# Performance work log

Hardware: AMD Instinct MI355X
Metric: run time of the kernel (lower is better)

The kernel has to match this reference:

```python
import jax, jax.numpy as jnp
import numpy as np
from jax import lax

HEADS, DIM_HEAD, LANDMARKS, PINV_ITERS = 8, 64, 256, 6
D = 512


def layernorm(x, w, b, eps=1e-5):
    mu = x.mean(-1, keepdims=True)
    var = ((x - mu) ** 2).mean(-1, keepdims=True)
    return (x - mu) * lax.rsqrt(var + eps) * w + b


def pinv_iter(x, iters=PINV_ITERS):
    # Moore-Penrose pseudo-inverse via Newton-Schulz (lucidrains nystrom-attention)
    abs_x = jnp.abs(x)
    z = jnp.swapaxes(x, -1, -2) / (jnp.max(abs_x.sum(-1)) * jnp.max(abs_x.sum(-2)))
    I = jnp.eye(x.shape[-1], dtype=x.dtype)
    for _ in range(iters):
        xz = x @ z
        z = 0.25 * z @ (13 * I - xz @ (15 * I - xz @ (7 * I - xz)))
    return z


def nystrom_attention(x, qkv_w, out_w, out_b, res_w):
    b, n, _ = x.shape
    m = LANDMARKS
    pad = (m - n % m) % m
    xp = jnp.pad(x, ((0, 0), (pad, 0), (0, 0)))  # left-pad seq to multiple of m
    n_p = n + pad
    q, k, v = jnp.split(xp @ qkv_w, 3, axis=-1)
    split = lambda t: t.reshape(b, n_p, HEADS, DIM_HEAD).transpose(0, 2, 1, 3)
    q, k, v = split(q), split(k), split(v)  # (b, h, n_p, d)
    q = q * DIM_HEAD ** -0.5
    l = n_p // m  # tokens per landmark
    q_l = q.reshape(b, HEADS, m, l, DIM_HEAD).mean(3)  # (b, h, m, d)
    k_l = k.reshape(b, HEADS, m, l, DIM_HEAD).mean(3)
    a1 = jax.nn.softmax(jnp.einsum('bhnd,bhmd->bhnm', q, k_l), -1)  # (b,h,n_p,m)
    a2 = jax.nn.softmax(jnp.einsum('bhmd,bhld->bhml', q_l, k_l), -1)  # (b,h,m,m)
    a3 = jax.nn.softmax(jnp.einsum('bhmd,bhnd->bhmn', q_l, k), -1)  # (b,h,m,n_p)
    out = (a1 @ pinv_iter(a2)) @ (a3 @ v)  # (b,h,n_p,d)
    # depthwise residual conv over the seq dim, kernel (33,1), one per head
    res = lax.conv_general_dilated(v, res_w, (1, 1), [(16, 16), (0, 0)],
                                   dimension_numbers=('NCHW', 'OIHW', 'NCHW'),
                                   feature_group_count=HEADS)
    out = out + res
    out = out.transpose(0, 2, 1, 3).reshape(b, n_p, HEADS * DIM_HEAD)
    return (out @ out_w + out_b)[:, -n:]


def ppeg(x, Hh, Ww, w7, b7, w5, b5, w3, b3):
    B, _, C = x.shape
    cls_tok, feat = x[:, :1], x[:, 1:]
    f = feat.transpose(0, 2, 1).reshape(B, C, Hh, Ww)
    def dwconv(w, bb, p):
        return lax.conv_general_dilated(f, w, (1, 1), [(p, p), (p, p)],
                                        dimension_numbers=('NCHW', 'OIHW', 'NCHW'),
                                        feature_group_count=C) + bb[None, :, None, None]
    y = f + dwconv(w7, b7, 3) + dwconv(w5, b5, 2) + dwconv(w3, b3, 1)
    y = y.reshape(B, C, Hh * Ww).transpose(0, 2, 1)
    return jnp.concatenate([cls_tok, y], axis=1)


def setup_inputs() -> dict:
    key = jax.random.key(0)
    ks = jax.random.split(key, 16)
    E, NC, H = 1024, 4, HEADS
    f32 = jnp.float32
    rn = lambda k, shp, s=0.02: (jax.random.normal(k, shp, f32) * s)
    return {
        'x': jax.random.normal(ks[0], (1, 40960, E), f32),
        'fc1_w': rn(ks[1], (E, D)), 'fc1_b': jnp.zeros((D,), f32),
        'cls_token': jax.random.normal(ks[2], (1, 1, D), f32),
        'l1_norm_w': jnp.ones((D,), f32), 'l1_norm_b': jnp.zeros((D,), f32),
        'l1_qkv_w': rn(ks[3], (D, 3 * D)),
        'l1_out_w': rn(ks[4], (D, D)), 'l1_out_b': jnp.zeros((D,), f32),
        'l1_res_w': rn(ks[5], (H, 1, 33, 1), 0.1),
        'ppeg_w7': rn(ks[6], (D, 1, 7, 7), 0.1), 'ppeg_b7': jnp.zeros((D,), f32),
        'ppeg_w5': rn(ks[7], (D, 1, 5, 5), 0.1), 'ppeg_b5': jnp.zeros((D,), f32),
        'ppeg_w3': rn(ks[8], (D, 1, 3, 3), 0.1), 'ppeg_b3': jnp.zeros((D,), f32),
        'l2_norm_w': jnp.ones((D,), f32), 'l2_norm_b': jnp.zeros((D,), f32),
        'l2_qkv_w': rn(ks[9], (D, 3 * D)),
        'l2_out_w': rn(ks[10], (D, D)), 'l2_out_b': jnp.zeros((D,), f32),
        'l2_res_w': rn(ks[11], (H, 1, 33, 1), 0.1),
        'norm_w': jnp.ones((D,), f32), 'norm_b': jnp.zeros((D,), f32),
        'fc3_w': rn(ks[12], (D, NC)), 'fc3_b': jnp.zeros((NC,), f32),
    }


def reference(x, fc1_w, fc1_b, cls_token, l1_norm_w, l1_norm_b, l1_qkv_w, l1_out_w, l1_out_b, l1_res_w, ppeg_w7, ppeg_b7, ppeg_w5, ppeg_b5, ppeg_w3, ppeg_b3, l2_norm_w, l2_norm_b, l2_qkv_w, l2_out_w, l2_out_b, l2_res_w, norm_w, norm_b, fc3_w, fc3_b):
    B, N, E = x.shape  # (1, 40960, 1024)
    POOL_OUT = 20480
    # AdaptiveMaxPool2d((20480, E)) on a (1, N, E) tensor: max-pool seq dim N -> 20480
    ft = x.reshape(B, POOL_OUT, N // POOL_OUT, E).max(axis=2)
    ft = jax.nn.relu(ft @ fc1_w + fc1_b)  # (1, 20480, 512)
    Hn = ft.shape[1]
    _H = int(np.ceil(np.sqrt(Hn)))  # 144
    add = _H * _H - Hn  # 256
    ft = jnp.concatenate([ft, ft[:, :add]], axis=1)  # (1, 20736, 512)
    h = jnp.concatenate([jnp.broadcast_to(cls_token, (B, 1, D)), ft], axis=1)  # 20737 tokens
    h = h + nystrom_attention(layernorm(h, l1_norm_w, l1_norm_b), l1_qkv_w, l1_out_w, l1_out_b, l1_res_w)
    h = ppeg(h, _H, _H, ppeg_w7, ppeg_b7, ppeg_w5, ppeg_b5, ppeg_w3, ppeg_b3)
    h = h + nystrom_attention(layernorm(h, l2_norm_w, l2_norm_b), l2_qkv_w, l2_out_w, l2_out_b, l2_res_w)
    h = layernorm(h, norm_w, norm_b)[:, 0]
    logits = h @ fc3_w + fc3_b
    return logits, jax.nn.softmax(logits, -1), jnp.argmax(logits, -1)
```

## Files before the change

kernel.cpp:

```cpp
#include <hip/hip_runtime.h>


constexpr int D_    = 512;
constexpr int E_    = 1024;
constexpr int NTOK  = 20737;
constexpr int NP_   = 20992;
constexpr int NH_   = 8;
constexpr int HD_   = 64;
constexpr int MLM   = 256;
constexpr int LCH   = 82;
constexpr int HHW   = 144;
constexpr int NFEAT = 20736;
constexpr int PADR  = 255;
constexpr int NCH   = 41;
constexpr int CHTOK = 512;

typedef __attribute__((ext_vector_type(8))) short bf16x8;
typedef __attribute__((ext_vector_type(4))) float f32x4;

__device__ __forceinline__ unsigned short f2bf(float f){
  unsigned int u = __float_as_uint(f);
  unsigned int r = u + 0x7fffu + ((u >> 16) & 1u);
  return (unsigned short)(r >> 16);
}
__device__ __forceinline__ float bfu(unsigned short u){
  return __uint_as_float((unsigned int)u << 16);
}

__device__ __forceinline__ float waveMaxF(float v){
#pragma unroll
  for (int o = 32; o > 0; o >>= 1) v = fmaxf(v, __shfl_xor(v, o));
  return v;
}
__device__ __forceinline__ float waveSumF(float v){
#pragma unroll
  for (int o = 32; o > 0; o >>= 1) v += __shfl_xor(v, o);
  return v;
}
__device__ __forceinline__ float blockMax256(float v, float* sbuf){
  v = waveMaxF(v);
  if ((threadIdx.x & 63) == 0) sbuf[threadIdx.x >> 6] = v;
  __syncthreads();
  float r = fmaxf(fmaxf(sbuf[0], sbuf[1]), fmaxf(sbuf[2], sbuf[3]));
  __syncthreads();
  return r;
}
__device__ __forceinline__ float blockSum256(float v, float* sbuf){
  v = waveSumF(v);
  if ((threadIdx.x & 63) == 0) sbuf[threadIdx.x >> 6] = v;
  __syncthreads();
  float r = sbuf[0] + sbuf[1] + sbuf[2] + sbuf[3];
  __syncthreads();
  return r;
}

__global__ __launch_bounds__(256) void wtrans_kernel(
    const float* __restrict__ W, unsigned short* __restrict__ Wt, int K, int N){
  __shared__ float tile[32][33];
  const int kb = blockIdx.x * 32, nb = blockIdx.y * 32;
  const int tx = threadIdx.x, ty = threadIdx.y;
  for (int i = ty; i < 32; i += 8) tile[i][tx] = W[(size_t)(kb + i) * N + nb + tx];
  __syncthreads();
  for (int i = ty; i < 32; i += 8)
    Wt[(size_t)(nb + i) * K + kb + tx] = f2bf(tile[tx][i]);
}

__global__ __launch_bounds__(256) void pool_bf16_kernel(
    const float* __restrict__ x, unsigned short* __restrict__ Ah){
  size_t idx4 = ((size_t)blockIdx.x * 256 + threadIdx.x) * 4;
  size_t m = idx4 >> 10, e = idx4 & 1023;
  float4 a = *(const float4*)(x + (m * 2) * E_ + e);
  float4 b = *(const float4*)(x + (m * 2 + 1) * E_ + e);
  unsigned long long pk =
      (unsigned long long)f2bf(fmaxf(a.x, b.x))
    | ((unsigned long long)f2bf(fmaxf(a.y, b.y)) << 16)
    | ((unsigned long long)f2bf(fmaxf(a.z, b.z)) << 32)
    | ((unsigned long long)f2bf(fmaxf(a.w, b.w)) << 48);
  *(unsigned long long*)(Ah + idx4) = pk;
}

__device__ __forceinline__ void mfma_tile128(
    const unsigned short* __restrict__ A, int arows, int bm,
    const unsigned short* __restrict__ Bt, int bn, int K,
    f32x4 acc[4][4], unsigned short* As, unsigned short* Bs){
  const int t = threadIdx.x;
  const int lane = t & 63, wave = t >> 6;
  const int wr = wave >> 1, wc = wave & 1;
  const int m16 = lane & 15, quad = lane >> 4;
  for (int kc = 0; kc < K; kc += 64){
    for (int idx = t; idx < 1024; idx += 256){
      int row = idx >> 3, off = (idx & 7) * 8;
      int ga = bm + row;
      ulonglong2 av = {0ull, 0ull};
      if (ga < arows) av = *(const ulonglong2*)(A + (size_t)ga * K + kc + off);
      *(ulonglong2*)(As + row * 72 + off) = av;
      ulonglong2 bv = *(const ulonglong2*)(Bt + (size_t)(bn + row) * K + kc + off);
      *(ulonglong2*)(Bs + row * 72 + off) = bv;
    }
    __syncthreads();
#pragma unroll
    for (int k2 = 0; k2 < 64; k2 += 32){
      bf16x8 af[4], bf[4];
#pragma unroll
      for (int mi = 0; mi < 4; mi++)
        af[mi] = *(const bf16x8*)(As + (wr * 64 + mi * 16 + m16) * 72 + k2 + quad * 8);
#pragma unroll
      for (int ni = 0; ni < 4; ni++)
        bf[ni] = *(const bf16x8*)(Bs + (wc * 64 + ni * 16 + m16) * 72 + k2 + quad * 8);
#pragma unroll
      for (int mi = 0; mi < 4; mi++)
#pragma unroll
        for (int ni = 0; ni < 4; ni++)
          acc[mi][ni] = __builtin_amdgcn_mfma_f32_16x16x32_bf16(af[mi], bf[ni], acc[mi][ni], 0, 0, 0);
    }
    __syncthreads();
  }
}

__global__ __launch_bounds__(256) void fc1_mfma_kernel(
    const unsigned short* __restrict__ Ah, const unsigned short* __restrict__ Bt,
    const float* __restrict__ bias, float* __restrict__ h){
  __shared__ unsigned short As[128 * 72], Bs[128 * 72];
  f32x4 z4 = {0.f, 0.f, 0.f, 0.f};
  f32x4 acc[4][4];
#pragma unroll
  for (int i = 0; i < 4; i++)
#pragma unroll
    for (int j = 0; j < 4; j++) acc[i][j] = z4;
  const int bm = blockIdx.x * 128, bn = blockIdx.y * 128;
  mfma_tile128(Ah, 20480, bm, Bt, bn, E_, acc, As, Bs);
  const int lane = threadIdx.x & 63, wave = threadIdx.x >> 6;
  const int wr = wave >> 1, wc = wave & 1;
  const int m16 = lane & 15, quad = lane >> 4;
#pragma unroll
  for (int mi = 0; mi < 4; mi++)
#pragma unroll
    for (int ni = 0; ni < 4; ni++){
      int col = bn + wc * 64 + ni * 16 + m16;
      float bv = bias[col];
#pragma unroll
      for (int r = 0; r < 4; r++){
        int row = bm + wr * 64 + mi * 16 + quad * 4 + r;
        float vv = fmaxf(acc[mi][ni][r] + bv, 0.f);
        h[(size_t)(1 + row) * D_ + col] = vv;
        if (row < 256) h[(size_t)(20481 + row) * D_ + col] = vv;
      }
    }
}

__global__ void cls_kernel(const float* __restrict__ cls, float* __restrict__ h){
  int c = blockIdx.x * 256 + threadIdx.x;
  if (c < D_) h[c] = cls[c];
}

__global__ void row0_copy_kernel(const float* __restrict__ src, float* __restrict__ dst){
  int c = blockIdx.x * 256 + threadIdx.x;
  if (c < D_) dst[c] = src[c];
}

__global__ __launch_bounds__(256) void ln_pad_kernel(
    const float* __restrict__ h, const float* __restrict__ w,
    const float* __restrict__ b, unsigned short* __restrict__ xph){
  const int r = blockIdx.x;
  const int t = threadIdx.x;
  if (r < PADR){
    xph[(size_t)r * D_ + t] = 0;
    xph[(size_t)r * D_ + 256 + t] = 0;
    return;
  }
  __shared__ float s4[4];
  const float* x = h + (size_t)(r - PADR) * D_;
  float a0 = x[t], a1 = x[t + 256];
  float mu = blockSum256(a0 + a1, s4) * (1.f / 512.f);
  float d0 = a0 - mu, d1 = a1 - mu;
  float var = blockSum256(d0 * d0 + d1 * d1, s4) * (1.f / 512.f);
  float rs = rsqrtf(var + 1e-5f);
  xph[(size_t)r * D_ + t]       = f2bf(d0 * rs * w[t] + b[t]);
  xph[(size_t)r * D_ + 256 + t] = f2bf(d1 * rs * w[t + 256] + b[t + 256]);
}

__global__ __launch_bounds__(256) void qkv_mfma_kernel(
    const unsigned short* __restrict__ A, const unsigned short* __restrict__ Bt,
    unsigned short* __restrict__ q16, unsigned short* __restrict__ k16,
    unsigned short* __restrict__ v16){
  __shared__ unsigned short As[128 * 72], Bs[128 * 72];
  f32x4 z4 = {0.f, 0.f, 0.f, 0.f};
  f32x4 acc[4][4];
#pragma unroll
  for (int i = 0; i < 4; i++)
#pragma unroll
    for (int j = 0; j < 4; j++) acc[i][j] = z4;
  const int bm = blockIdx.x * 128, bn = blockIdx.y * 128;
  mfma_tile128(A, NP_, bm, Bt, bn, D_, acc, As, Bs);
  const int lane = threadIdx.x & 63, wave = threadIdx.x >> 6;
  const int wr = wave >> 1, wc = wave & 1;
  const int m16 = lane & 15, quad = lane >> 4;
#pragma unroll
  for (int mi = 0; mi < 4; mi++)
#pragma unroll
    for (int ni = 0; ni < 4; ni++){
      int col = bn + wc * 64 + ni * 16 + m16;
      int which = col >> 9, hh = (col >> 6) & 7, d = col & 63;
      size_t cbase = (size_t)hh * NP_ * HD_ + d;
      unsigned short* dst;
      float sc = 1.f;
      if (which == 0){ dst = q16; sc = 0.125f; }
      else if (which == 1) dst = k16;
      else dst = v16;
#pragma unroll
      for (int r = 0; r < 4; r++){
        int row = bm + wr * 64 + mi * 16 + quad * 4 + r;
        dst[cbase + (size_t)row * HD_] = f2bf(acc[mi][ni][r] * sc);
      }
    }
}

__global__ __launch_bounds__(64) void landmark_kernel(
    const unsigned short* __restrict__ q16, const unsigned short* __restrict__ k16,
    float* __restrict__ ql, float* __restrict__ kl,
    unsigned short* __restrict__ qlh, unsigned short* __restrict__ klh){
  const int im = blockIdx.x, h = blockIdx.y, d = threadIdx.x;
  size_t base = ((size_t)h * NP_ + (size_t)im * LCH) * HD_ + d;
  float sq = 0.f, sk = 0.f;
  for (int r = 0; r < LCH; r++){
    sq += bfu(q16[base + (size_t)r * HD_]);
    sk += bfu(k16[base + (size_t)r * HD_]);
  }
  float qm = sq * (1.f / 82.f), km = sk * (1.f / 82.f);
  size_t oidx = ((size_t)h * MLM + im) * HD_ + d;
  ql[oidx] = qm;  qlh[oidx] = f2bf(qm);
  kl[oidx] = km;  klh[oidx] = f2bf(km);
}

__global__ __launch_bounds__(256) void a2_kernel(
    const float* __restrict__ ql, const float* __restrict__ kl,
    float* __restrict__ a2){
  const int im = blockIdx.x, h = blockIdx.y, t = threadIdx.x;
  __shared__ __align__(16) float qs[64];
  __shared__ float s4[4];
  if (t < 64) qs[t] = ql[((size_t)h * MLM + im) * HD_ + t];
  __syncthreads();
  const float4* kr4 = (const float4*)(kl + ((size_t)h * MLM + t) * HD_);
  const float4* qs4 = (const float4*)qs;
  float s = 0.f;
#pragma unroll
  for (int d4 = 0; d4 < 16; d4++){
    float4 kv = kr4[d4], qv = qs4[d4];
    s += qv.x*kv.x + qv.y*kv.y + qv.z*kv.z + qv.w*kv.w;
  }
  float mx = blockMax256(s, s4);
  float e = __expf(s - mx);
  float S = blockSum256(e, s4);
  a2[((size_t)h * MLM + im) * MLM + t] = e / S;
}

__global__ __launch_bounds__(256) void pinv_scale_kernel(
    const float* __restrict__ a2, float* __restrict__ scal){
  const int h = blockIdx.x, j = threadIdx.x;
  const float* A = a2 + (size_t)h * MLM * MLM;
  float rs = 0.f, cs = 0.f;
  for (int t = 0; t < MLM; t++){
    rs += fabsf(A[(size_t)j * MLM + t]);
    cs += fabsf(A[(size_t)t * MLM + j]);
  }
  __shared__ float s4[4];
  float rmax = blockMax256(rs, s4);
  float cmax = blockMax256(cs, s4);
  if (j == 0){ scal[h * 2] = rmax; scal[h * 2 + 1] = cmax; }
}

__global__ __launch_bounds__(256) void pinv_init_kernel(
    const float* __restrict__ a2, const float* __restrict__ scal,
    float* __restrict__ z){
  const int i = blockIdx.x, h = blockIdx.y, j = threadIdx.x;
  float rmax = scal[0], cmax = scal[1];
#pragma unroll
  for (int hh = 1; hh < 8; hh++){
    rmax = fmaxf(rmax, scal[hh * 2]);
    cmax = fmaxf(cmax, scal[hh * 2 + 1]);
  }
  float inv = 1.f / (rmax * cmax);
  z[((size_t)h * MLM + i) * MLM + j] = a2[((size_t)h * MLM + j) * MLM + i] * inv;
}

__global__ __launch_bounds__(256) void bmm256_mfma_kernel(
    const float* __restrict__ Ab, const float* __restrict__ Bb,
    float* __restrict__ Cb, float c0, float sgn, float c1){
  __shared__ unsigned short Ash[64 * 40], Asl[64 * 40];
  __shared__ unsigned short Bsh[64 * 40], Bsl[64 * 40];
  const int h = blockIdx.z;
  const float* A = Ab + (size_t)h * 65536;
  const float* B = Bb + (size_t)h * 65536;
  float* C = Cb + (size_t)h * 65536;
  const int bm = blockIdx.x * 64, bn = blockIdx.y * 64;
  const int t = threadIdx.x, lane = t & 63, w = t >> 6;
  const int wr = w >> 1, wc = w & 1, m16 = lane & 15, quad = lane >> 4;
  f32x4 z4 = {0.f, 0.f, 0.f, 0.f};
  f32x4 acc[2][2] = {{z4, z4}, {z4, z4}};
  for (int kc = 0; kc < 256; kc += 32){
    {
      int row = t >> 2, c8 = (t & 3) * 8;
      const float* src = A + (size_t)(bm + row) * 256 + kc + c8;
      float xs[8];
      *(float4*)(xs)     = *(const float4*)src;
      *(float4*)(xs + 4) = *(const float4*)(src + 4);
#pragma unroll
      for (int j = 0; j < 8; j++){
        unsigned short hi = f2bf(xs[j]);
        Ash[row * 40 + c8 + j] = hi;
        Asl[row * 40 + c8 + j] = f2bf(xs[j] - bfu(hi));
      }
      int k = t >> 3, n8 = (t & 7) * 8;
      const float* bsrc = B + (size_t)(kc + k) * 256 + bn + n8;
      float ys[8];
      *(float4*)(ys)     = *(const float4*)bsrc;
      *(float4*)(ys + 4) = *(const float4*)(bsrc + 4);
#pragma unroll
      for (int j = 0; j < 8; j++){
        float xv = sgn * ys[j];
        if (kc + k == bn + n8 + j) xv += c0;
        unsigned short hi = f2bf(xv);
        Bsh[(n8 + j) * 40 + k] = hi;
        Bsl[(n8 + j) * 40 + k] = f2bf(xv - bfu(hi));
      }
    }
    __syncthreads();
    bf16x8 ah[2], al[2], bh[2], bl[2];
#pragma unroll
    for (int mi = 0; mi < 2; mi++){
      ah[mi] = *(const bf16x8*)(Ash + (wr * 32 + mi * 16 + m16) * 40 + quad * 8);
      al[mi] = *(const bf16x8*)(Asl + (wr * 32 + mi * 16 + m16) * 40 + quad * 8);
      bh[mi] = *(const bf16x8*)(Bsh + (wc * 32 + mi * 16 + m16) * 40 + quad * 8);
      bl[mi] = *(const bf16x8*)(Bsl + (wc * 32 + mi * 16 + m16) * 40 + quad * 8);
    }
#pragma unroll
    for (int mi = 0; mi < 2; mi++)
#pragma unroll
      for (int ni = 0; ni < 2; ni++){
        acc[mi][ni] = __builtin_amdgcn_mfma_f32_16x16x32_bf16(ah[mi], bh[ni], acc[mi][ni], 0, 0, 0);
        acc[mi][ni] = __builtin_amdgcn_mfma_f32_16x16x32_bf16(ah[mi], bl[ni], acc[mi][ni], 0, 0, 0);
        acc[mi][ni] = __builtin_amdgcn_mfma_f32_16x16x32_bf16(al[mi], bh[ni], acc[mi][ni], 0, 0, 0);
      }
    __syncthreads();
  }
#pragma unroll
  for (int mi = 0; mi < 2; mi++)
#pragma unroll
    for (int ni = 0; ni < 2; ni++)
#pragma unroll
      for (int r = 0; r < 4; r++){
        int row = bm + wr * 32 + mi * 16 + quad * 4 + r;
        int col = bn + wc * 32 + ni * 16 + m16;
        C[(size_t)row * 256 + col] = c1 * acc[mi][ni][r];
      }
}

__global__ __launch_bounds__(256) void a3v_part_kernel(
    const unsigned short* __restrict__ qlh, const unsigned short* __restrict__ k16,
    const unsigned short* __restrict__ v16, float* __restrict__ pacc,
    float* __restrict__ pml){
  __shared__ __align__(16) unsigned short qs16[64 * 72];
  __shared__ __align__(16) unsigned short kb16[64 * 72];
  __shared__ __align__(16) unsigned short vt16[64 * 72];
  const int lt = blockIdx.x, h = blockIdx.y, ch = blockIdx.z;
  const int t = threadIdx.x;
  const int lane = t & 63, w = t >> 6;
  const int m16 = lane & 15, quad = lane >> 4;

  const unsigned short* qg = qlh + ((size_t)h * MLM + lt * 64) * HD_;
  for (int idx = t; idx < 512; idx += 256){
    int row = idx >> 3, off = (idx & 7) * 8;
    *(uint4*)(qs16 + row * 72 + off) = *(const uint4*)(qg + (size_t)row * HD_ + off);
  }
  f32x4 z4 = {0.f, 0.f, 0.f, 0.f};
  f32x4 acc_o[4] = {z4, z4, z4, z4};
  float mreg[4], lreg[4];
#pragma unroll
  for (int r = 0; r < 4; r++){ mreg[r] = -3.0e38f; lreg[r] = 0.f; }
  const unsigned short* kg = k16 + ((size_t)h * NP_ + ch * CHTOK) * HD_;
  const unsigned short* vg = v16 + ((size_t)h * NP_ + ch * CHTOK) * HD_;

  for (int sc = 0; sc < 8; sc++){
    __syncthreads();
    for (int idx = t; idx < 512; idx += 256){
      int row = idx >> 3, off = (idx & 7) * 8;
      *(uint4*)(kb16 + row * 72 + off) =
          *(const uint4*)(kg + (size_t)(sc * 64 + row) * HD_ + off);
      uint4 pv = *(const uint4*)(vg + (size_t)(sc * 64 + row) * HD_ + off);
      unsigned int uu[4] = {pv.x, pv.y, pv.z, pv.w};
#pragma unroll
      for (int j = 0; j < 4; j++){
        vt16[(off + 2 * j)     * 72 + row] = (unsigned short)(uu[j] & 0xffffu);
        vt16[(off + 2 * j + 1) * 72 + row] = (unsigned short)(uu[j] >> 16);
      }
    }
    __syncthreads();
    f32x4 acc_s[4] = {z4, z4, z4, z4};
#pragma unroll
    for (int kc = 0; kc < 64; kc += 32){
      bf16x8 a = *(const bf16x8*)(qs16 + (w * 16 + m16) * 72 + kc + quad * 8);
#pragma unroll
      for (int ni = 0; ni < 4; ni++){
        bf16x8 b = *(const bf16x8*)(kb16 + (ni * 16 + m16) * 72 + kc + quad * 8);
        acc_s[ni] = __builtin_amdgcn_mfma_f32_16x16x32_bf16(a, b, acc_s[ni], 0, 0, 0);
      }
    }
    __syncthreads();
#pragma unroll
    for (int r = 0; r < 4; r++){
      float cm = fmaxf(fmaxf(acc_s[0][r], acc_s[1][r]), fmaxf(acc_s[2][r], acc_s[3][r]));
#pragma unroll
      for (int o = 1; o < 16; o <<= 1) cm = fmaxf(cm, __shfl_xor(cm, o));
      float mn = fmaxf(mreg[r], cm);
      float scl = __expf(mreg[r] - mn);
      float p0 = __expf(acc_s[0][r] - mn), p1 = __expf(acc_s[1][r] - mn);
      float p2 = __expf(acc_s[2][r] - mn), p3 = __expf(acc_s[3][r] - mn);
      float ls = (p0 + p1) + (p2 + p3);
#pragma unroll
      for (int o = 1; o < 16; o <<= 1) ls += __shfl_xor(ls, o);
      lreg[r] = lreg[r] * scl + ls;
      mreg[r] = mn;
      acc_o[0][r] *= scl; acc_o[1][r] *= scl;
      acc_o[2][r] *= scl; acc_o[3][r] *= scl;
      int prow = (w * 16 + quad * 4 + r) * 72 + m16;
      kb16[prow + 0]  = f2bf(p0);
      kb16[prow + 16] = f2bf(p1);
      kb16[prow + 32] = f2bf(p2);
      kb16[prow + 48] = f2bf(p3);
    }
    __syncthreads();
#pragma unroll
    for (int kc = 0; kc < 64; kc += 32){
      bf16x8 a = *(const bf16x8*)(kb16 + (w * 16 + m16) * 72 + kc + quad * 8);
#pragma unroll
      for (int ni = 0; ni < 4; ni++){
        bf16x8 b = *(const bf16x8*)(vt16 + (ni * 16 + m16) * 72 + kc + quad * 8);
        acc_o[ni] = __builtin_amdgcn_mfma_f32_16x16x32_bf16(a, b, acc_o[ni], 0, 0, 0);
      }
    }
  }
#pragma unroll
  for (int r = 0; r < 4; r++){
    int im = lt * 64 + w * 16 + quad * 4 + r;
    size_t base = ((size_t)h * NCH + ch) * MLM + im;
#pragma unroll
    for (int ni = 0; ni < 4; ni++)
      pacc[base * HD_ + ni * 16 + m16] = acc_o[ni][r];
    if (m16 == 0){
      pml[base * 2]     = mreg[r];
      pml[base * 2 + 1] = lreg[r];
    }
  }
}

__global__ __launch_bounds__(64) void a3v_combine_kernel(
    const float* __restrict__ pacc, const float* __restrict__ pml,
    float* __restrict__ t1){
  const int im = blockIdx.x, h = blockIdx.y, lane = threadIdx.x;
  float M = -3.0e38f;
  for (int c = 0; c < NCH; c++)
    M = fmaxf(M, pml[(((size_t)h * NCH + c) * MLM + im) * 2]);
  float accv = 0.f, L = 0.f;
  for (int c = 0; c < NCH; c++){
    size_t base = ((size_t)h * NCH + c) * MLM + im;
    float mc = pml[base * 2], lc = pml[base * 2 + 1];
    float w = __expf(mc - M);
    accv += w * pacc[base * HD_ + lane];
    L += w * lc;
  }
  t1[((size_t)h * MLM + im) * HD_ + lane] = accv / L;
}

__global__ __launch_bounds__(256) void zt1_kernel(
    const float* __restrict__ z, const float* __restrict__ t1,
    unsigned short* __restrict__ t2t){
  const int h = blockIdx.y;
  const int t = threadIdx.x;
  const int d = t & 63, ri = t >> 6;
  const int im = blockIdx.x * 4 + ri;
  const float* zr = z + ((size_t)h * MLM + im) * MLM;
  const float* t1h = t1 + (size_t)h * MLM * HD_;
  float acc = 0.f;
#pragma unroll 8
  for (int kk = 0; kk < MLM; kk++) acc += zr[kk] * t1h[(size_t)kk * HD_ + d];
  t2t[((size_t)h * HD_ + d) * MLM + im] = f2bf(acc);
}

__global__ __launch_bounds__(256) void out_tile_kernel(
    const unsigned short* __restrict__ q16, const unsigned short* __restrict__ klh,
    const unsigned short* __restrict__ t2t, const unsigned short* __restrict__ v16,
    const float* __restrict__ resw, unsigned short* __restrict__ outh){
  __shared__ __align__(16) unsigned short smem[64 * 72 * 2 + 64 * 264];
  unsigned short* qs16 = smem;
  unsigned short* kb16 = smem + 64 * 72;
  unsigned short* Ps   = smem + 64 * 72 * 2;
  const int tile = blockIdx.x, h = blockIdx.y;
  const int n0 = PADR + tile * 64;
  const int t = threadIdx.x;
  const int lane = t & 63, w = t >> 6;
  const int m16 = lane & 15, quad = lane >> 4;

  {
    const unsigned short* qh = q16 + (size_t)h * NP_ * HD_;
    for (int idx = t; idx < 512; idx += 256){
      int row = idx >> 3, off = (idx & 7) * 8;
      int n = n0 + row;
      uint4 val = {0u, 0u, 0u, 0u};
      if (n < NP_) val = *(const uint4*)(qh + (size_t)n * HD_ + off);
      *(uint4*)(qs16 + row * 72 + off) = val;
    }
  }
  f32x4 z4 = {0.f, 0.f, 0.f, 0.f};
  f32x4 acc_s[16];
#pragma unroll
  for (int i = 0; i < 16; i++) acc_s[i] = z4;
  const unsigned short* klg = klh + (size_t)h * MLM * HD_;
  for (int m = 0; m < 4; m++){
    __syncthreads();
    for (int idx = t; idx < 512; idx += 256){
      int row = idx >> 3, off = (idx & 7) * 8;
      *(uint4*)(kb16 + row * 72 + off) =
          *(const uint4*)(klg + (size_t)(m * 64 + row) * HD_ + off);
    }
    __syncthreads();
#pragma unroll
    for (int kc = 0; kc < 64; kc += 32){
      bf16x8 a = *(const bf16x8*)(qs16 + (w * 16 + m16) * 72 + kc + quad * 8);
#pragma unroll
      for (int ni = 0; ni < 4; ni++){
        bf16x8 b = *(const bf16x8*)(kb16 + (ni * 16 + m16) * 72 + kc + quad * 8);
        acc_s[m * 4 + ni] = __builtin_amdgcn_mfma_f32_16x16x32_bf16(a, b, acc_s[m * 4 + ni], 0, 0, 0);
      }
    }
  }
  __syncthreads();
#pragma unroll
  for (int r = 0; r < 4; r++){
    float mx = acc_s[0][r];
#pragma unroll
    for (int mc = 1; mc < 16; mc++) mx = fmaxf(mx, acc_s[mc][r]);
#pragma unroll
    for (int o = 1; o < 16; o <<= 1) mx = fmaxf(mx, __shfl_xor(mx, o));
    float p[16]; float sum = 0.f;
#pragma unroll
    for (int mc = 0; mc < 16; mc++){ p[mc] = __expf(acc_s[mc][r] - mx); sum += p[mc]; }
#pragma unroll
    for (int o = 1; o < 16; o <<= 1) sum += __shfl_xor(sum, o);
    float inv = 1.f / sum;
    int prow = (w * 16 + quad * 4 + r) * 264;
#pragma unroll
    for (int mc = 0; mc < 16; mc++)
      Ps[prow + (mc >> 2) * 64 + (mc & 3) * 16 + m16] = f2bf(p[mc] * inv);
  }
  f32x4 acc_o[4] = {z4, z4, z4, z4};
  const unsigned short* t2g = t2t + (size_t)h * HD_ * MLM;
  for (int ch = 0; ch < 4; ch++){
    __syncthreads();
    {
      int row = t >> 2, c8 = (t & 3) * 16;
      const unsigned short* src = t2g + (size_t)row * MLM + ch * 64 + c8;
      *(uint4*)(kb16 + row * 72 + c8)     = *(const uint4*)src;
      *(uint4*)(kb16 + row * 72 + c8 + 8) = *(const uint4*)(src + 8);
    }
    __syncthreads();
#pragma unroll
    for (int kc = 0; kc < 64; kc += 32){
      bf16x8 a = *(const bf16x8*)(Ps + (w * 16 + m16) * 264 + ch * 64 + kc + quad * 8);
#pragma unroll
      for (int ni = 0; ni < 4; ni++){
        bf16x8 b = *(const bf16x8*)(kb16 + (ni * 16 + m16) * 72 + kc + quad * 8);
        acc_o[ni] = __builtin_amdgcn_mfma_f32_16x16x32_bf16(a, b, acc_o[ni], 0, 0, 0);
      }
    }
  }
  __syncthreads();
  float* Obuf = (float*)Ps;
  unsigned short* vtile = (unsigned short*)(Obuf + 64 * 66);
#pragma unroll
  for (int r = 0; r < 4; r++){
    int row = w * 16 + quad * 4 + r;
#pragma unroll
    for (int ni = 0; ni < 4; ni++)
      Obuf[row * 66 + ni * 16 + m16] = acc_o[ni][r];
  }
  {
    const unsigned short* vh = v16 + (size_t)h * NP_ * HD_;
    for (int idx = t; idx < 768; idx += 256){
      int row = idx >> 3, off = (idx & 7) * 8;
      int nn = n0 - 16 + row;
      uint4 val = {0u, 0u, 0u, 0u};
      if (nn < NP_) val = *(const uint4*)(vh + (size_t)nn * HD_ + off);
      *(uint4*)(vtile + row * 72 + off) = val;
    }
  }
  __syncthreads();
  float wreg[33];
  {
    const float* wr = resw + h * 33;
#pragma unroll
    for (int kk = 0; kk < 33; kk++) wreg[kk] = wr[kk];
  }
  const int ty = t >> 4, tx = t & 15;
#pragma unroll
  for (int i = 0; i < 4; i++){
    int lrow = ty * 4 + i;
    float c0v = 0.f, c1v = 0.f, c2v = 0.f, c3v = 0.f;
    for (int kk = 0; kk < 33; kk++){
      uint2 uv = *(const uint2*)(vtile + (lrow + kk) * 72 + tx * 4);
      float wv = wreg[kk];
      c0v += __uint_as_float(uv.x << 16) * wv;
      c1v += __uint_as_float(uv.x & 0xffff0000u) * wv;
      c2v += __uint_as_float(uv.y << 16) * wv;
      c3v += __uint_as_float(uv.y & 0xffff0000u) * wv;
    }
    int trow = tile * 64 + lrow;
    if (trow < NTOK){
      const float* orow = Obuf + lrow * 66 + tx * 4;
      unsigned long long pk =
          (unsigned long long)f2bf(orow[0] + c0v)
        | ((unsigned long long)f2bf(orow[1] + c1v) << 16)
        | ((unsigned long long)f2bf(orow[2] + c2v) << 32)
        | ((unsigned long long)f2bf(orow[3] + c3v) << 48);
      *(unsigned long long*)(outh + (size_t)trow * D_ + h * HD_ + tx * 4) = pk;
    }
  }
}

__global__ __launch_bounds__(256) void proj_mfma_kernel(
    const unsigned short* __restrict__ A, const unsigned short* __restrict__ Bt,
    const float* __restrict__ bias, float* __restrict__ h){
  __shared__ unsigned short As[128 * 72], Bs[128 * 72];
  f32x4 z4 = {0.f, 0.f, 0.f, 0.f};
  f32x4 acc[4][4];
#pragma unroll
  for (int i = 0; i < 4; i++)
#pragma unroll
    for (int j = 0; j < 4; j++) acc[i][j] = z4;
  const int bm = blockIdx.x * 128, bn = blockIdx.y * 128;
  mfma_tile128(A, NTOK, bm, Bt, bn, D_, acc, As, Bs);
  const int lane = threadIdx.x & 63, wave = threadIdx.x >> 6;
  const int wr = wave >> 1, wc = wave & 1;
  const int m16 = lane & 15, quad = lane >> 4;
#pragma unroll
  for (int mi = 0; mi < 4; mi++)
#pragma unroll
    for (int ni = 0; ni < 4; ni++){
      int col = bn + wc * 64 + ni * 16 + m16;
      float bv = bias[col];
#pragma unroll
      for (int r = 0; r < 4; r++){
        int row = bm + wr * 64 + mi * 16 + quad * 4 + r;
        if (row < NTOK) h[(size_t)row * D_ + col] += acc[mi][ni][r] + bv;
      }
    }
}

__global__ __launch_bounds__(512) void ppeg_combine_kernel(
    const float* __restrict__ w7, const float* __restrict__ b7,
    const float* __restrict__ w5, const float* __restrict__ b5,
    const float* __restrict__ w3, const float* __restrict__ b3,
    float* __restrict__ wcomb, float* __restrict__ bcomb){
  const int c = threadIdx.x;
#pragma unroll
  for (int i = 0; i < 7; i++){
#pragma unroll
    for (int j = 0; j < 7; j++){
      int di = i - 3, dj = j - 3;
      float wv = w7[(size_t)c * 49 + i * 7 + j];
      if (di >= -2 && di <= 2 && dj >= -2 && dj <= 2)
        wv += w5[(size_t)c * 25 + (di + 2) * 5 + (dj + 2)];
      if (di >= -1 && di <= 1 && dj >= -1 && dj <= 1)
        wv += w3[(size_t)c * 9 + (di + 1) * 3 + (dj + 1)];
      if (di == 0 && dj == 0) wv += 1.f;
      wcomb[(size_t)(i * 7 + j) * 512 + c] = wv;
    }
  }
  bcomb[c] = b7[c] + b5[c] + b3[c];
}

__global__ __launch_bounds__(512) void ppeg_conv_kernel(
    const float* __restrict__ h, const float* __restrict__ wcomb,
    const float* __restrict__ bcomb, float* __restrict__ h2){
  const int c = threadIdx.x;
  const int y = blockIdx.y;
  const int x0 = blockIdx.x * 8;
  float wc[49];
#pragma unroll
  for (int kk = 0; kk < 49; kk++) wc[kk] = wcomb[(size_t)kk * 512 + c];
  float acc[8];
  const float bv = bcomb[c];
#pragma unroll
  for (int p = 0; p < 8; p++) acc[p] = bv;
#pragma unroll
  for (int i = 0; i < 7; i++){
    const int yy = y + i - 3;
    if (yy < 0 || yy >= HHW) continue;
    const float* hrow = h + (size_t)(1 + yy * HHW) * D_ + c;
    float line[14];
#pragma unroll
    for (int j = 0; j < 14; j++){
      const int xx = x0 + j - 3;
      line[j] = (xx >= 0 && xx < HHW) ? hrow[(size_t)xx * D_] : 0.f;
    }
#pragma unroll
    for (int p = 0; p < 8; p++)
#pragma unroll
      for (int j = 0; j < 7; j++)
        acc[p] += line[p + j] * wc[i * 7 + j];
  }
#pragma unroll
  for (int p = 0; p < 8; p++)
    h2[(size_t)(1 + y * HHW + x0 + p) * D_ + c] = acc[p];
}

__global__ __launch_bounds__(512) void final_kernel(
    const float* __restrict__ h, const float* __restrict__ w,
    const float* __restrict__ b, const float* __restrict__ fc3w,
    const float* __restrict__ fc3b, float* __restrict__ out){
  __shared__ float vec[512];
  __shared__ float s8[8];
  __shared__ float lg[4];
  const int t = threadIdx.x;
  float x = h[t];
  float v = waveSumF(x);
  if ((t & 63) == 0) s8[t >> 6] = v;
  __syncthreads();
  float sum = 0.f;
#pragma unroll
  for (int i = 0; i < 8; i++) sum += s8[i];
  float mu = sum * (1.f / 512.f);
  __syncthreads();
  float d = x - mu;
  v = waveSumF(d * d);
  if ((t & 63) == 0) s8[t >> 6] = v;
  __syncthreads();
  float var = 0.f;
#pragma unroll
  for (int i = 0; i < 8; i++) var += s8[i];
  var *= (1.f / 512.f);
  float rs = rsqrtf(var + 1e-5f);
  vec[t] = d * rs * w[t] + b[t];
  __syncthreads();
  if (t < 4){
    float acc = fc3b[t];
    for (int kk = 0; kk < 512; kk++) acc += vec[kk] * fc3w[kk * 4 + t];
    lg[t] = acc;
  }
  __syncthreads();
  if (t == 0){
    float m = fmaxf(fmaxf(lg[0], lg[1]), fmaxf(lg[2], lg[3]));
    float e[4], se = 0.f;
#pragma unroll
    for (int i = 0; i < 4; i++){ e[i] = __expf(lg[i] - m); se += e[i]; }
    int am = 0; float bm = lg[0];
#pragma unroll
    for (int i = 1; i < 4; i++) if (lg[i] > bm){ bm = lg[i]; am = i; }
#pragma unroll
    for (int i = 0; i < 4; i++){ out[i] = lg[i]; out[4 + i] = e[i] / se; }
    out[8] = (float)am;
  }
}

extern "C" void kernel_launch(void* const* d_in, const int* in_sizes, int n_in,
                              void* d_out, int out_size, void* d_ws, size_t ws_size,
                              hipStream_t stream) {
  const float* x       = (const float*)d_in[0];
  const float* fc1_w   = (const float*)d_in[1];
  const float* fc1_b   = (const float*)d_in[2];
  const float* cls_tok = (const float*)d_in[3];
  const float* l1_nw   = (const float*)d_in[4];
  const float* l1_nb   = (const float*)d_in[5];
  const float* l1_qkvw = (const float*)d_in[6];
  const float* l1_outw = (const float*)d_in[7];
  const float* l1_outb = (const float*)d_in[8];
  const float* l1_resw = (const float*)d_in[9];
  const float* ppeg_w7 = (const float*)d_in[10];
  const float* ppeg_b7 = (const float*)d_in[11];
  const float* ppeg_w5 = (const float*)d_in[12];
  const float* ppeg_b5 = (const float*)d_in[13];
  const float* ppeg_w3 = (const float*)d_in[14];
  const float* ppeg_b3 = (const float*)d_in[15];
  const float* l2_nw   = (const float*)d_in[16];
  const float* l2_nb   = (const float*)d_in[17];
  const float* l2_qkvw = (const float*)d_in[18];
  const float* l2_outw = (const float*)d_in[19];
  const float* l2_outb = (const float*)d_in[20];
  const float* l2_resw = (const float*)d_in[21];
  const float* norm_w  = (const float*)d_in[22];
  const float* norm_b  = (const float*)d_in[23];
  const float* fc3_w   = (const float*)d_in[24];
  const float* fc3_b   = (const float*)d_in[25];

  float* W = (float*)d_ws;
  size_t o = 0;
  float* hbuf = W + o; o += (size_t)NTOK * D_;
  float* xp   = W + o; o += (size_t)NP_ * D_;
  float* qb   = W + o; o += (size_t)NH_ * NP_ * HD_;
  float* kb   = W + o; o += (size_t)NH_ * NP_ * HD_;
  float* vb   = W + o; o += (size_t)NH_ * NP_ * HD_;
  float* qlb  = W + o; o += (size_t)NH_ * MLM * HD_;
  float* klb  = W + o; o += (size_t)NH_ * MLM * HD_;
  float* a2b  = W + o; o += (size_t)NH_ * MLM * MLM;
  float* z0   = W + o; o += (size_t)NH_ * MLM * MLM;
  float* z1   = W + o; o += (size_t)NH_ * MLM * MLM;
  float* ta   = W + o; o += (size_t)NH_ * MLM * MLM;
  float* tb   = W + o; o += (size_t)NH_ * MLM * MLM;
  float* tc   = W + o; o += (size_t)NH_ * MLM * MLM;
  float* t1b  = W + o; o += (size_t)NH_ * MLM * HD_;
  float* t2r  = W + o; o += (size_t)NH_ * MLM * HD_;
  float* scalf = W + o; o += 16;
  float* wcomb = W + o; o += 49 * 512;
  float* bcomb = W + o; o += 512;
  unsigned short* fc1_wt  = (unsigned short*)(W + o); o += (size_t)D_ * E_ / 2;
  unsigned short* qkv_wt1 = (unsigned short*)(W + o); o += (size_t)1536 * D_ / 2;
  unsigned short* qkv_wt2 = (unsigned short*)(W + o); o += (size_t)1536 * D_ / 2;
  unsigned short* out_wt1 = (unsigned short*)(W + o); o += (size_t)D_ * D_ / 2;
  unsigned short* out_wt2 = (unsigned short*)(W + o); o += (size_t)D_ * D_ / 2;
  unsigned short* qlh = (unsigned short*)(W + o); o += (size_t)NH_ * MLM * HD_ / 2;
  unsigned short* klh = (unsigned short*)(W + o); o += (size_t)NH_ * MLM * HD_ / 2;
  float* hbuf2 = W + o; o += (size_t)NTOK * D_;

  unsigned short* xph = (unsigned short*)xp;
  float* pacc = xp;
  float* pml  = xp + (size_t)NH_ * NCH * MLM * HD_;
  unsigned short* outh = (unsigned short*)xp;
  unsigned short* Ah  = (unsigned short*)qb;
  unsigned short* q16 = (unsigned short*)qb;
  unsigned short* k16 = (unsigned short*)kb;
  unsigned short* v16 = (unsigned short*)vb;
  unsigned short* t2t = (unsigned short*)t2r;

  wtrans_kernel<<<dim3(E_ / 32, D_ / 32), dim3(32, 8), 0, stream>>>(fc1_w, fc1_wt, E_, D_);
  wtrans_kernel<<<dim3(D_ / 32, 1536 / 32), dim3(32, 8), 0, stream>>>(l1_qkvw, qkv_wt1, D_, 1536);
  wtrans_kernel<<<dim3(D_ / 32, 1536 / 32), dim3(32, 8), 0, stream>>>(l2_qkvw, qkv_wt2, D_, 1536);
  wtrans_kernel<<<dim3(D_ / 32, D_ / 32), dim3(32, 8), 0, stream>>>(l1_outw, out_wt1, D_, D_);
  wtrans_kernel<<<dim3(D_ / 32, D_ / 32), dim3(32, 8), 0, stream>>>(l2_outw, out_wt2, D_, D_);
  ppeg_combine_kernel<<<1, 512, 0, stream>>>(ppeg_w7, ppeg_b7, ppeg_w5, ppeg_b5,
                                             ppeg_w3, ppeg_b3, wcomb, bcomb);

  pool_bf16_kernel<<<20480, 256, 0, stream>>>(x, Ah);
  fc1_mfma_kernel<<<dim3(160, 4), 256, 0, stream>>>(Ah, fc1_wt, fc1_b, hbuf);
  cls_kernel<<<2, 256, 0, stream>>>(cls_tok, hbuf);

  auto run_layer = [&](float* hcur, const float* nw, const float* nb,
                       const unsigned short* qkvwt, const unsigned short* outwt,
                       const float* outb, const float* resw){
    ln_pad_kernel<<<NP_, 256, 0, stream>>>(hcur, nw, nb, xph);
    qkv_mfma_kernel<<<dim3(164, 12), 256, 0, stream>>>(xph, qkvwt, q16, k16, v16);
    landmark_kernel<<<dim3(256, 8), 64, 0, stream>>>(q16, k16, qlb, klb, qlh, klh);
    a2_kernel<<<dim3(256, 8), 256, 0, stream>>>(qlb, klb, a2b);
    pinv_scale_kernel<<<8, 256, 0, stream>>>(a2b, scalf);
    pinv_init_kernel<<<dim3(256, 8), 256, 0, stream>>>(a2b, scalf, z0);
    float* zc = z0; float* za = z1;
    for (int it = 0; it < 6; it++){
      bmm256_mfma_kernel<<<dim3(4, 4, 8), 256, 0, stream>>>(a2b, zc, ta, 0.f, 1.f, 1.f);
      bmm256_mfma_kernel<<<dim3(4, 4, 8), 256, 0, stream>>>(ta, ta, tb, 7.f, -1.f, 1.f);
      bmm256_mfma_kernel<<<dim3(4, 4, 8), 256, 0, stream>>>(ta, tb, tc, 15.f, -1.f, 1.f);
      bmm256_mfma_kernel<<<dim3(4, 4, 8), 256, 0, stream>>>(zc, tc, za, 13.f, -1.f, 0.25f);
      float* tswap = zc; zc = za; za = tswap;
    }
    a3v_part_kernel<<<dim3(4, 8, NCH), 256, 0, stream>>>(qlh, k16, v16, pacc, pml);
    a3v_combine_kernel<<<dim3(256, 8), 64, 0, stream>>>(pacc, pml, t1b);
    zt1_kernel<<<dim3(64, 8), 256, 0, stream>>>(zc, t1b, t2t);
    out_tile_kernel<<<dim3(325, 8), 256, 0, stream>>>(q16, klh, t2t, v16, resw, outh);
    proj_mfma_kernel<<<dim3(163, 4), 256, 0, stream>>>(outh, outwt, outb, hcur);
  };

  run_layer(hbuf, l1_nw, l1_nb, qkv_wt1, out_wt1, l1_outb, l1_resw);
  ppeg_conv_kernel<<<dim3(HHW / 8, HHW), 512, 0, stream>>>(hbuf, wcomb, bcomb, hbuf2);
  row0_copy_kernel<<<2, 256, 0, stream>>>(hbuf, hbuf2);
  run_layer(hbuf2, l2_nw, l2_nb, qkv_wt2, out_wt2, l2_outb, l2_resw);
  final_kernel<<<1, 512, 0, stream>>>(hbuf2, norm_w, norm_b, fc3_w, fc3_b, (float*)d_out);
}
```

Baseline: 1.700 ms.

## Store pinv operands pre-split as bf16 hi/lo in transposed layout

The Newton-Schulz matmul kernel now reads pre-split bf16 hi/lo operands, with B stored transposed, and copies them straight into shared memory with vector loads. This removes the per-tile fp32-to-bf16 splitting and the strided transpose writes in the bmm. Each producer kernel now emits both row-major and negated-transposed split copies, so the sign flip and diagonal shift are folded into the layout. Separately, the a3v online softmax skips the rescale when no row max increases. The cost is more workspace and extra output writes per bmm.

```diff
diff --git a/kernel.cpp b/kernel.cpp
--- a/kernel.cpp
+++ b/kernel.cpp
@@ -234,7 +234,8 @@
 
 __global__ __launch_bounds__(256) void a2_kernel(
     const float* __restrict__ ql, const float* __restrict__ kl,
-    float* __restrict__ a2){
+    float* __restrict__ a2, unsigned short* __restrict__ a2h,
+    unsigned short* __restrict__ a2l){
   const int im = blockIdx.x, h = blockIdx.y, t = threadIdx.x;
   __shared__ __align__(16) float qs[64];
   __shared__ float s4[4];
@@ -251,7 +252,12 @@
   float mx = blockMax256(s, s4);
   float e = __expf(s - mx);
   float S = blockSum256(e, s4);
-  a2[((size_t)h * MLM + im) * MLM + t] = e / S;
+  float v = e / S;
+  size_t idx = ((size_t)h * MLM + im) * MLM + t;
+  a2[idx] = v;
+  unsigned short hi = f2bf(v);
+  a2h[idx] = hi;
+  a2l[idx] = f2bf(v - bfu(hi));
 }
 
 __global__ __launch_bounds__(256) void pinv_scale_kernel(
@@ -271,7 +277,8 @@
 
 __global__ __launch_bounds__(256) void pinv_init_kernel(
     const float* __restrict__ a2, const float* __restrict__ scal,
-    float* __restrict__ z){
+    unsigned short* __restrict__ zh, unsigned short* __restrict__ zl,
+    unsigned short* __restrict__ zth, unsigned short* __restrict__ ztl){
   const int i = blockIdx.x, h = blockIdx.y, j = threadIdx.x;
   float rmax = scal[0], cmax = scal[1];
 #pragma unroll
@@ -280,67 +287,79 @@
     cmax = fmaxf(cmax, scal[hh * 2 + 1]);
   }
   float inv = 1.f / (rmax * cmax);
-  z[((size_t)h * MLM + i) * MLM + j] = a2[((size_t)h * MLM + j) * MLM + i] * inv;
-}
-
-__global__ __launch_bounds__(256) void bmm256_mfma_kernel(
-    const float* __restrict__ Ab, const float* __restrict__ Bb,
-    float* __restrict__ Cb, float c0, float sgn, float c1){
-  __shared__ unsigned short Ash[64 * 40], Asl[64 * 40];
-  __shared__ unsigned short Bsh[64 * 40], Bsl[64 * 40];
+  size_t idx = ((size_t)h * MLM + i) * MLM + j;
+  float vr = a2[((size_t)h * MLM + j) * MLM + i] * inv;
+  float vt = a2[idx] * inv;
+  unsigned short hi = f2bf(vr);
+  zh[idx] = hi; zl[idx] = f2bf(vr - bfu(hi));
+  hi = f2bf(vt);
+  zth[idx] = hi; ztl[idx] = f2bf(vt - bfu(hi));
+}
+
+__global__ __launch_bounds__(256) void bmm256_split_kernel(
+    const unsigned short* __restrict__ Ahg, const unsigned short* __restrict__ Alg,
+    const unsigned short* __restrict__ Bthg, const unsigned short* __restrict__ Btlg,
+    float c0, float c1,
+    unsigned short* __restrict__ Crh, unsigned short* __restrict__ Crl,
+    unsigned short* __restrict__ Cth, unsigned short* __restrict__ Ctl,
+    float* __restrict__ Cf, unsigned int tsgn){
+  __shared__ __align__(16) unsigned short Ash[64 * 72], Asl[64 * 72];
+  __shared__ __align__(16) unsigned short Bsh[64 * 72], Bsl[64 * 72];
   const int h = blockIdx.z;
-  const float* A = Ab + (size_t)h * 65536;
-  const float* B = Bb + (size_t)h * 65536;
-  float* C = Cb + (size_t)h * 65536;
   const int bm = blockIdx.x * 64, bn = blockIdx.y * 64;
   const int t = threadIdx.x, lane = t & 63, w = t >> 6;
   const int wr = w >> 1, wc = w & 1, m16 = lane & 15, quad = lane >> 4;
+  const size_t hb = (size_t)h * 65536;
+  const unsigned short* gAh0 = Ahg + hb + (size_t)bm * 256;
+  const unsigned short* gAl0 = Alg + hb + (size_t)bm * 256;
+  const unsigned short* gBh0 = Bthg + hb + (size_t)bn * 256;
+  const unsigned short* gBl0 = Btlg + hb + (size_t)bn * 256;
   f32x4 z4 = {0.f, 0.f, 0.f, 0.f};
   f32x4 acc[2][2] = {{z4, z4}, {z4, z4}};
-  for (int kc = 0; kc < 256; kc += 32){
+  for (int kc = 0; kc < 256; kc += 64){
     {
-      int row = t >> 2, c8 = (t & 3) * 8;
-      const float* src = A + (size_t)(bm + row) * 256 + kc + c8;
-      float xs[8];
-      *(float4*)(xs)     = *(const float4*)src;
-      *(float4*)(xs + 4) = *(const float4*)(src + 4);
-#pragma unroll
-      for (int j = 0; j < 8; j++){
-        unsigned short hi = f2bf(xs[j]);
-        Ash[row * 40 + c8 + j] = hi;
-        Asl[row * 40 + c8 + j] = f2bf(xs[j] - bfu(hi));
-      }
-      int k = t >> 3, n8 = (t & 7) * 8;
-      const float* bsrc = B + (size_t)(kc + k) * 256 + bn + n8;
-      float ys[8];
-      *(float4*)(ys)     = *(const float4*)bsrc;
-      *(float4*)(ys + 4) = *(const float4*)(bsrc + 4);
-#pragma unroll
-      for (int j = 0; j < 8; j++){
-        float xv = sgn * ys[j];
-        if (kc + k == bn + n8 + j) xv += c0;
-        unsigned short hi = f2bf(xv);
-        Bsh[(n8 + j) * 40 + k] = hi;
-        Bsl[(n8 + j) * 40 + k] = f2bf(xv - bfu(hi));
-      }
-    }
-    __syncthreads();
-    bf16x8 ah[2], al[2], bh[2], bl[2];
-#pragma unroll
-    for (int mi = 0; mi < 2; mi++){
-      ah[mi] = *(const bf16x8*)(Ash + (wr * 32 + mi * 16 + m16) * 40 + quad * 8);
-      al[mi] = *(const bf16x8*)(Asl + (wr * 32 + mi * 16 + m16) * 40 + quad * 8);
-      bh[mi] = *(const bf16x8*)(Bsh + (wc * 32 + mi * 16 + m16) * 40 + quad * 8);
-      bl[mi] = *(const bf16x8*)(Bsl + (wc * 32 + mi * 16 + m16) * 40 + quad * 8);
-    }
-#pragma unroll
-    for (int mi = 0; mi < 2; mi++)
-#pragma unroll
-      for (int ni = 0; ni < 2; ni++){
-        acc[mi][ni] = __builtin_amdgcn_mfma_f32_16x16x32_bf16(ah[mi], bh[ni], acc[mi][ni], 0, 0, 0);
-        acc[mi][ni] = __builtin_amdgcn_mfma_f32_16x16x32_bf16(ah[mi], bl[ni], acc[mi][ni], 0, 0, 0);
-        acc[mi][ni] = __builtin_amdgcn_mfma_f32_16x16x32_bf16(al[mi], bh[ni], acc[mi][ni], 0, 0, 0);
-      }
+      int row = t >> 3, o8 = (t & 7) * 8;
+      size_t g0 = (size_t)row * 256 + kc + o8;
+      size_t g1 = g0 + 32 * 256;
+      int l0 = row * 72 + o8, l1 = l0 + 32 * 72;
+      *(uint4*)(Ash + l0) = *(const uint4*)(gAh0 + g0);
+      *(uint4*)(Ash + l1) = *(const uint4*)(gAh0 + g1);
+      *(uint4*)(Asl + l0) = *(const uint4*)(gAl0 + g0);
+      *(uint4*)(Asl + l1) = *(const uint4*)(gAl0 + g1);
+      *(uint4*)(Bsh + l0) = *(const uint4*)(gBh0 + g0);
+      *(uint4*)(Bsh + l1) = *(const uint4*)(gBh0 + g1);
+      *(uint4*)(Bsl + l0) = *(const uint4*)(gBl0 + g0);
+      *(uint4*)(Bsl + l1) = *(const uint4*)(gBl0 + g1);
+    }
+    __syncthreads();
+    if (c0 != 0.f && kc == bn){
+      if (t < 64){
+        float v = c0 + bfu(Bsh[t * 72 + t]) + bfu(Bsl[t * 72 + t]);
+        unsigned short hi = f2bf(v);
+        Bsh[t * 72 + t] = hi;
+        Bsl[t * 72 + t] = f2bf(v - bfu(hi));
+      }
+      __syncthreads();
+    }
+#pragma unroll
+    for (int k2 = 0; k2 < 64; k2 += 32){
+      bf16x8 ah[2], al[2], bh[2], bl[2];
+#pragma unroll
+      for (int mi = 0; mi < 2; mi++){
+        ah[mi] = *(const bf16x8*)(Ash + (wr * 32 + mi * 16 + m16) * 72 + k2 + quad * 8);
+        al[mi] = *(const bf16x8*)(Asl + (wr * 32 + mi * 16 + m16) * 72 + k2 + quad * 8);
+        bh[mi] = *(const bf16x8*)(Bsh + (wc * 32 + mi * 16 + m16) * 72 + k2 + quad * 8);
+        bl[mi] = *(const bf16x8*)(Bsl + (wc * 32 + mi * 16 + m16) * 72 + k2 + quad * 8);
+      }
+#pragma unroll
+      for (int mi = 0; mi < 2; mi++)
+#pragma unroll
+        for (int ni = 0; ni < 2; ni++){
+          acc[mi][ni] = __builtin_amdgcn_mfma_f32_16x16x32_bf16(ah[mi], bh[ni], acc[mi][ni], 0, 0, 0);
+          acc[mi][ni] = __builtin_amdgcn_mfma_f32_16x16x32_bf16(ah[mi], bl[ni], acc[mi][ni], 0, 0, 0);
+          acc[mi][ni] = __builtin_amdgcn_mfma_f32_16x16x32_bf16(al[mi], bh[ni], acc[mi][ni], 0, 0, 0);
+        }
+    }
     __syncthreads();
   }
 #pragma unroll
@@ -351,7 +370,17 @@
       for (int r = 0; r < 4; r++){
         int row = bm + wr * 32 + mi * 16 + quad * 4 + r;
         int col = bn + wc * 32 + ni * 16 + m16;
-        C[(size_t)row * 256 + col] = c1 * acc[mi][ni][r];
+        float v = c1 * acc[mi][ni][r];
+        unsigned short hi = f2bf(v);
+        unsigned short lo = f2bf(v - bfu(hi));
+        size_t rm = hb + (size_t)row * 256 + col;
+        if (Crh){ Crh[rm] = hi; Crl[rm] = lo; }
+        if (Cth){
+          size_t tm = hb + (size_t)col * 256 + row;
+          Cth[tm] = hi ^ (unsigned short)tsgn;
+          Ctl[tm] = lo ^ (unsigned short)tsgn;
+        }
+        if (Cf) Cf[rm] = v;
       }
 }
 
@@ -411,17 +440,21 @@
       float cm = fmaxf(fmaxf(acc_s[0][r], acc_s[1][r]), fmaxf(acc_s[2][r], acc_s[3][r]));
 #pragma unroll
       for (int o = 1; o < 16; o <<= 1) cm = fmaxf(cm, __shfl_xor(cm, o));
-      float mn = fmaxf(mreg[r], cm);
-      float scl = __expf(mreg[r] - mn);
-      float p0 = __expf(acc_s[0][r] - mn), p1 = __expf(acc_s[1][r] - mn);
-      float p2 = __expf(acc_s[2][r] - mn), p3 = __expf(acc_s[3][r] - mn);
+      if (__any(cm > mreg[r])){
+        float mn = fmaxf(mreg[r], cm);
+        float scl = __expf(mreg[r] - mn);
+        lreg[r] *= scl;
+        acc_o[0][r] *= scl; acc_o[1][r] *= scl;
+        acc_o[2][r] *= scl; acc_o[3][r] *= scl;
+        mreg[r] = mn;
+      }
+      float mcur = mreg[r];
+      float p0 = __expf(acc_s[0][r] - mcur), p1 = __expf(acc_s[1][r] - mcur);
+      float p2 = __expf(acc_s[2][r] - mcur), p3 = __expf(acc_s[3][r] - mcur);
       float ls = (p0 + p1) + (p2 + p3);
 #pragma unroll
       for (int o = 1; o < 16; o <<= 1) ls += __shfl_xor(ls, o);
-      lreg[r] = lreg[r] * scl + ls;
-      mreg[r] = mn;
-      acc_o[0][r] *= scl; acc_o[1][r] *= scl;
-      acc_o[2][r] *= scl; acc_o[3][r] *= scl;
+      lreg[r] += ls;
       int prow = (w * 16 + quad * 4 + r) * 72 + m16;
       kb16[prow + 0]  = f2bf(p0);
       kb16[prow + 16] = f2bf(p1);
@@ -801,11 +834,7 @@
   float* qlb  = W + o; o += (size_t)NH_ * MLM * HD_;
   float* klb  = W + o; o += (size_t)NH_ * MLM * HD_;
   float* a2b  = W + o; o += (size_t)NH_ * MLM * MLM;
-  float* z0   = W + o; o += (size_t)NH_ * MLM * MLM;
-  float* z1   = W + o; o += (size_t)NH_ * MLM * MLM;
-  float* ta   = W + o; o += (size_t)NH_ * MLM * MLM;
-  float* tb   = W + o; o += (size_t)NH_ * MLM * MLM;
-  float* tc   = W + o; o += (size_t)NH_ * MLM * MLM;
+  float* zfin = W + o; o += (size_t)NH_ * MLM * MLM;
   float* t1b  = W + o; o += (size_t)NH_ * MLM * HD_;
   float* t2r  = W + o; o += (size_t)NH_ * MLM * HD_;
   float* scalf = W + o; o += 16;
@@ -818,6 +847,25 @@
   unsigned short* out_wt2 = (unsigned short*)(W + o); o += (size_t)D_ * D_ / 2;
   unsigned short* qlh = (unsigned short*)(W + o); o += (size_t)NH_ * MLM * HD_ / 2;
   unsigned short* klh = (unsigned short*)(W + o); o += (size_t)NH_ * MLM * HD_ / 2;
+  const size_t HM = (size_t)NH_ * MLM * MLM;
+  unsigned short* usp = (unsigned short*)(W + o); o += 18 * HM / 2;
+  unsigned short* a2sh  = usp; usp += HM;
+  unsigned short* a2sl  = usp; usp += HM;
+  unsigned short* tah_s = usp; usp += HM;
+  unsigned short* tal_s = usp; usp += HM;
+  unsigned short* tath_s = usp; usp += HM;
+  unsigned short* tatl_s = usp; usp += HM;
+  unsigned short* tbth_s = usp; usp += HM;
+  unsigned short* tbtl_s = usp; usp += HM;
+  unsigned short* tcth_s = usp; usp += HM;
+  unsigned short* tctl_s = usp; usp += HM;
+  unsigned short* zsh[2], *zsl[2], *zsth[2], *zstl[2];
+  for (int s = 0; s < 2; s++){
+    zsh[s]  = usp; usp += HM;
+    zsl[s]  = usp; usp += HM;
+    zsth[s] = usp; usp += HM;
+    zstl[s] = usp; usp += HM;
+  }
   float* hbuf2 = W + o; o += (size_t)NTOK * D_;
 
   unsigned short* xph = (unsigned short*)xp;
@@ -848,20 +896,30 @@
     ln_pad_kernel<<<NP_, 256, 0, stream>>>(hcur, nw, nb, xph);
     qkv_mfma_kernel<<<dim3(164, 12), 256, 0, stream>>>(xph, qkvwt, q16, k16, v16);
     landmark_kernel<<<dim3(256, 8), 64, 0, stream>>>(q16, k16, qlb, klb, qlh, klh);
-    a2_kernel<<<dim3(256, 8), 256, 0, stream>>>(qlb, klb, a2b);
+    a2_kernel<<<dim3(256, 8), 256, 0, stream>>>(qlb, klb, a2b, a2sh, a2sl);
     pinv_scale_kernel<<<8, 256, 0, stream>>>(a2b, scalf);
-    pinv_init_kernel<<<dim3(256, 8), 256, 0, stream>>>(a2b, scalf, z0);
-    float* zc = z0; float* za = z1;
+    pinv_init_kernel<<<dim3(256, 8), 256, 0, stream>>>(a2b, scalf,
+        zsh[0], zsl[0], zsth[0], zstl[0]);
+    int c = 0;
     for (int it = 0; it < 6; it++){
-      bmm256_mfma_kernel<<<dim3(4, 4, 8), 256, 0, stream>>>(a2b, zc, ta, 0.f, 1.f, 1.f);
-      bmm256_mfma_kernel<<<dim3(4, 4, 8), 256, 0, stream>>>(ta, ta, tb, 7.f, -1.f, 1.f);
-      bmm256_mfma_kernel<<<dim3(4, 4, 8), 256, 0, stream>>>(ta, tb, tc, 15.f, -1.f, 1.f);
-      bmm256_mfma_kernel<<<dim3(4, 4, 8), 256, 0, stream>>>(zc, tc, za, 13.f, -1.f, 0.25f);
-      float* tswap = zc; zc = za; za = tswap;
+      bmm256_split_kernel<<<dim3(4, 4, 8), 256, 0, stream>>>(
+          a2sh, a2sl, zsth[c], zstl[c], 0.f, 1.f,
+          tah_s, tal_s, tath_s, tatl_s, nullptr, 0x8000u);
+      bmm256_split_kernel<<<dim3(4, 4, 8), 256, 0, stream>>>(
+          tah_s, tal_s, tath_s, tatl_s, 7.f, 1.f,
+          nullptr, nullptr, tbth_s, tbtl_s, nullptr, 0x8000u);
+      bmm256_split_kernel<<<dim3(4, 4, 8), 256, 0, stream>>>(
+          tah_s, tal_s, tbth_s, tbtl_s, 15.f, 1.f,
+          nullptr, nullptr, tcth_s, tctl_s, nullptr, 0x8000u);
+      bmm256_split_kernel<<<dim3(4, 4, 8), 256, 0, stream>>>(
+          zsh[c], zsl[c], tcth_s, tctl_s, 13.f, 0.25f,
+          zsh[c ^ 1], zsl[c ^ 1], zsth[c ^ 1], zstl[c ^ 1],
+          (it == 5) ? zfin : nullptr, 0u);
+      c ^= 1;
     }
     a3v_part_kernel<<<dim3(4, 8, NCH), 256, 0, stream>>>(qlh, k16, v16, pacc, pml);
     a3v_combine_kernel<<<dim3(256, 8), 64, 0, stream>>>(pacc, pml, t1b);
-    zt1_kernel<<<dim3(64, 8), 256, 0, stream>>>(zc, t1b, t2t);
+    zt1_kernel<<<dim3(64, 8), 256, 0, stream>>>(zfin, t1b, t2t);
     out_tile_kernel<<<dim3(325, 8), 256, 0, stream>>>(q16, klh, t2t, v16, resw, outh);
     proj_mfma_kernel<<<dim3(163, 4), 256, 0, stream>>>(outh, outwt, outb, hcur);
   };
```

Measured after the change: 1.673 ms. About the same (-1.5%).
